# Optimization experiments

Measured on AMD Instinct MI355X. Metric: run time of the kernel, lower is better.

The kernel has to match this reference:

```python
import jax, jax.numpy as jnp
import numpy as np


def _ln(x, g, b):
    m = x.mean(-1, keepdims=True)
    v = x.var(-1, keepdims=True)
    return (x - m) * jax.lax.rsqrt(v + 1e-5) * g + b


def _shift(x):
    # RWKV time-shift: xx[t] = x[t-1], xx[0] = 0
    return jnp.pad(x, ((0, 0), (1, 0), (0, 0)))[:, :-1]


def setup_inputs() -> dict:
    key = jax.random.key(0)
    ks = jax.random.split(key, 20)
    B, S, D, E, F = 2, 2048, 1024, 8, 2048
    s = 0.02
    return dict(
        x=jax.random.normal(ks[0], (B, S, D), jnp.float32),
        ln1_g=jnp.ones((D,), jnp.float32), ln1_b=jnp.zeros((D,), jnp.float32),
        ln2_g=jnp.ones((D,), jnp.float32), ln2_b=jnp.zeros((D,), jnp.float32),
        tm_mu_k=jax.random.uniform(ks[1], (D,), jnp.float32),
        tm_mu_v=jax.random.uniform(ks[2], (D,), jnp.float32),
        tm_mu_r=jax.random.uniform(ks[3], (D,), jnp.float32),
        time_decay=jax.random.normal(ks[4], (D,), jnp.float32) * 0.1,
        time_first=jax.random.normal(ks[5], (D,), jnp.float32) * 0.1,
        Wk=jax.random.normal(ks[6], (D, D), jnp.float32) * s,
        Wv=jax.random.normal(ks[7], (D, D), jnp.float32) * s,
        Wr=jax.random.normal(ks[8], (D, D), jnp.float32) * s,
        Wo=jax.random.normal(ks[9], (D, D), jnp.float32) * s,
        router_w=jax.random.normal(ks[10], (D, E), jnp.float32) * s,
        cm_mu_k=jax.random.uniform(ks[11], (E, D), jnp.float32),
        cm_mu_r=jax.random.uniform(ks[12], (E, D), jnp.float32),
        eWk=jax.random.normal(ks[13], (E, D, F), jnp.float32) * s,
        eWv=jax.random.normal(ks[14], (E, F, D), jnp.float32) * s,
        eWr=jax.random.normal(ks[15], (E, D, D), jnp.float32) * s,
    )


def reference(x, ln1_g, ln1_b, ln2_g, ln2_b, tm_mu_k, tm_mu_v, tm_mu_r,
              time_decay, time_first, Wk, Wv, Wr, Wo, router_w,
              cm_mu_k, cm_mu_r, eWk, eWv, eWr):
    TOP_K = 2
    E = router_w.shape[1]
    B, S, D = x.shape

    # ---- TimeMix on ln1(x) ----
    xn = _ln(x, ln1_g, ln1_b)
    xx = _shift(xn)
    xk = xn * tm_mu_k + xx * (1.0 - tm_mu_k)
    xv = xn * tm_mu_v + xx * (1.0 - tm_mu_v)
    xr = xn * tm_mu_r + xx * (1.0 - tm_mu_r)
    k = xk @ Wk  # [B,S,D]
    v = xv @ Wv
    r = jax.nn.sigmoid(xr @ Wr)

    w = -jnp.exp(time_decay)  # per-channel decay < 0
    u = time_first

    def step(carry, kv_t):
        aa, bb, pp = carry
        kt, vt = kv_t
        qq = jnp.maximum(pp, u + kt)
        e1 = jnp.exp(pp - qq)
        e2 = jnp.exp(u + kt - qq)
        wkv_t = (e1 * aa + e2 * vt) / (e1 * bb + e2)
        qq2 = jnp.maximum(pp + w, kt)
        e1b = jnp.exp(pp + w - qq2)
        e2b = jnp.exp(kt - qq2)
        return (e1b * aa + e2b * vt, e1b * bb + e2b, qq2), wkv_t

    init = (jnp.zeros((B, D), x.dtype), jnp.zeros((B, D), x.dtype),
            jnp.full((B, D), -1e30, x.dtype))
    _, wkv = jax.lax.scan(step, init,
                          (k.transpose(1, 0, 2), v.transpose(1, 0, 2)))
    wkv = wkv.transpose(1, 0, 2)  # [B,S,D]
    x = x + (r * wkv) @ Wo  # residual

    # ---- Router on ln2(x) ----
    ei = _ln(x, ln2_g, ln2_b)
    probs = jax.nn.softmax(ei @ router_w, axis=-1)  # [B,S,E]
    vals, idx = jax.lax.top_k(probs, TOP_K)
    wts = vals / vals.sum(-1, keepdims=True)
    # dense per-token per-expert combine weight [B,S,E]
    tw = jnp.sum(jax.nn.one_hot(idx, E, dtype=x.dtype) * wts[..., None], axis=-2)

    # ---- Dense per-expert ChannelMix (every expert over full tensor) ----
    exx = _shift(ei)
    mk = cm_mu_k[:, None, None, :]  # [E,1,1,D]
    mr = cm_mu_r[:, None, None, :]
    xk_e = ei[None] * mk + exx[None] * (1.0 - mk)  # [E,B,S,D]
    xr_e = ei[None] * mr + exx[None] * (1.0 - mr)
    k_e = jnp.square(jax.nn.relu(jnp.einsum('ebsd,edf->ebsf', xk_e, eWk)))
    kv_e = jnp.einsum('ebsf,efd->ebsd', k_e, eWv)
    r_e = jax.nn.sigmoid(jnp.einsum('ebsd,edg->ebsg', xr_e, eWr))
    expert_out = r_e * kv_e  # [E,B,S,D]
    moe = jnp.einsum('ebsd,bse->bsd', expert_out, tw)
    return x + moe
```

## Files before the change

kernel.cpp:

```cpp
#include <hip/hip_runtime.h>
#include <hip/hip_bf16.h>
#include <stdint.h>

#define DEVI __device__ __forceinline__

typedef __attribute__((ext_vector_type(4))) float f32x4;
typedef __attribute__((ext_vector_type(8))) short short8;
typedef __attribute__((ext_vector_type(4))) short s16x4;

constexpr int B_ = 2, S_ = 2048, D_ = 1024, E_ = 8, F_ = 2048;
constexpr int M_ = B_ * S_;
constexpr int PC_ = 10240;
constexpr int NC_ = 64, L_ = 32;
constexpr int HB_ = 16;
constexpr size_t MD_ = (size_t)M_ * D_;
constexpr size_t DD_ = (size_t)D_ * D_;

DEVI short f2bf(float f) {
  uint32_t u = __float_as_uint(f);
  u = (u + 0x7fffu + ((u >> 16) & 1u)) >> 16;
  return (short)u;
}
DEVI float bf2f(short s) { return __uint_as_float(((uint32_t)(uint16_t)s) << 16); }
struct BfPair { short hi, lo; };
DEVI BfPair split2(float f) {
  BfPair p;
  p.hi = f2bf(f);
  p.lo = f2bf(f - bf2f(p.hi));
  return p;
}

DEVI void gload_lds16(const void* g, void* l) {
  __builtin_amdgcn_global_load_lds(
      (const __attribute__((address_space(1))) unsigned int*)g,
      (__attribute__((address_space(3))) unsigned int*)l, 16, 0, 0);
}

DEVI int swz(int row, int slot) { return slot ^ ((row >> 1) & 3); }

#define MFMA(a, b, c) __builtin_amdgcn_mfma_f32_16x16x32_bf16((a), (b), (c), 0, 0, 0)

__global__ __launch_bounds__(256) void lnmix_kernel(
    const float* __restrict__ x, const float* __restrict__ g,
    const float* __restrict__ b, const float* __restrict__ muk,
    const float* __restrict__ muv, const float* __restrict__ mur,
    short* __restrict__ xk, short* __restrict__ xv, short* __restrict__ xr) {
  int row = blockIdx.x;
  int tx = threadIdx.x;
  int s = row & (S_ - 1);
  size_t o = (size_t)row * D_ + tx * 4;
  f32x4 cur = *(const f32x4*)(x + o);
  f32x4 prv = {0.f, 0.f, 0.f, 0.f};
  if (s > 0) prv = *(const f32x4*)(x + o - D_);
  float a0 = cur[0] + cur[1] + cur[2] + cur[3];
  float a1 = cur[0] * cur[0] + cur[1] * cur[1] + cur[2] * cur[2] + cur[3] * cur[3];
  float a2 = prv[0] + prv[1] + prv[2] + prv[3];
  float a3 = prv[0] * prv[0] + prv[1] * prv[1] + prv[2] * prv[2] + prv[3] * prv[3];
#pragma unroll
  for (int o2 = 32; o2; o2 >>= 1) {
    a0 += __shfl_down(a0, o2);
    a1 += __shfl_down(a1, o2);
    a2 += __shfl_down(a2, o2);
    a3 += __shfl_down(a3, o2);
  }
  __shared__ float rd[4][4];
  if ((tx & 63) == 0) {
    rd[tx >> 6][0] = a0; rd[tx >> 6][1] = a1;
    rd[tx >> 6][2] = a2; rd[tx >> 6][3] = a3;
  }
  __syncthreads();
  a0 = rd[0][0] + rd[1][0] + rd[2][0] + rd[3][0];
  a1 = rd[0][1] + rd[1][1] + rd[2][1] + rd[3][1];
  a2 = rd[0][2] + rd[1][2] + rd[2][2] + rd[3][2];
  a3 = rd[0][3] + rd[1][3] + rd[2][3] + rd[3][3];
  float mc = a0 * (1.0f / D_);
  float rc = rsqrtf(a1 * (1.0f / D_) - mc * mc + 1e-5f);
  float mp = a2 * (1.0f / D_);
  float rp = rsqrtf(a3 * (1.0f / D_) - mp * mp + 1e-5f);
  int d = tx * 4;
  f32x4 gg = *(const f32x4*)(g + d);
  f32x4 bb = *(const f32x4*)(b + d);
  f32x4 mk = *(const f32x4*)(muk + d);
  f32x4 mv = *(const f32x4*)(muv + d);
  f32x4 mr = *(const f32x4*)(mur + d);
  s16x4 okh, okl, ovh, ovl, orh, orl;
#pragma unroll
  for (int j = 0; j < 4; j++) {
    float c = (cur[j] - mc) * rc * gg[j] + bb[j];
    float p = (s > 0) ? (prv[j] - mp) * rp * gg[j] + bb[j] : 0.f;
    BfPair pk = split2(c * mk[j] + p * (1.f - mk[j]));
    BfPair pv = split2(c * mv[j] + p * (1.f - mv[j]));
    BfPair pr = split2(c * mr[j] + p * (1.f - mr[j]));
    okh[j] = pk.hi; okl[j] = pk.lo;
    ovh[j] = pv.hi; ovl[j] = pv.lo;
    orh[j] = pr.hi; orl[j] = pr.lo;
  }
  *(s16x4*)(xk + o) = okh;
  *(s16x4*)(xk + MD_ + o) = okl;
  *(s16x4*)(xv + o) = ovh;
  *(s16x4*)(xv + MD_ + o) = ovl;
  *(s16x4*)(xr + o) = orh;
  *(s16x4*)(xr + MD_ + o) = orl;
}

__global__ __launch_bounds__(256) void ln2_router(
    const float* __restrict__ x, const float* __restrict__ P,
    const float* __restrict__ g, const float* __restrict__ b,
    const float* __restrict__ rw, float* __restrict__ xout,
    float* __restrict__ ei, int* __restrict__ idx2, float* __restrict__ wts2) {
  int row = blockIdx.x;
  int tx = threadIdx.x;
  size_t o = (size_t)row * D_ + tx * 4;
  f32x4 v = *(const f32x4*)(x + o);
  f32x4 p0 = *(const f32x4*)(P + o);
  f32x4 p1 = *(const f32x4*)(P + MD_ + o);
#pragma unroll
  for (int j = 0; j < 4; j++) v[j] += p0[j] + p1[j];
  *(f32x4*)(xout + o) = v;
  float s = v[0] + v[1] + v[2] + v[3];
  float s2 = v[0] * v[0] + v[1] * v[1] + v[2] * v[2] + v[3] * v[3];
#pragma unroll
  for (int of = 32; of; of >>= 1) {
    s += __shfl_down(s, of);
    s2 += __shfl_down(s2, of);
  }
  __shared__ float w1[4], w2[4];
  if ((tx & 63) == 0) { w1[tx >> 6] = s; w2[tx >> 6] = s2; }
  __syncthreads();
  s = w1[0] + w1[1] + w1[2] + w1[3];
  s2 = w2[0] + w2[1] + w2[2] + w2[3];
  float mean = s * (1.0f / D_);
  float rstd = rsqrtf(s2 * (1.0f / D_) - mean * mean + 1e-5f);
  f32x4 gg = *(const f32x4*)(g + tx * 4);
  f32x4 bb = *(const f32x4*)(b + tx * 4);
  f32x4 oo;
#pragma unroll
  for (int j = 0; j < 4; j++) oo[j] = (v[j] - mean) * rstd * gg[j] + bb[j];
  *(f32x4*)(ei + o) = oo;
  float pl[8] = {};
  const float* rr = rw + (size_t)(tx * 4) * 8;
#pragma unroll
  for (int j = 0; j < 4; j++)
#pragma unroll
    for (int e = 0; e < 8; e++) pl[e] += oo[j] * rr[j * 8 + e];
#pragma unroll
  for (int of = 32; of; of >>= 1)
#pragma unroll
    for (int e = 0; e < 8; e++) pl[e] += __shfl_down(pl[e], of);
  __shared__ float plw[4][8];
  if ((tx & 63) == 0)
#pragma unroll
    for (int e = 0; e < 8; e++) plw[tx >> 6][e] = pl[e];
  __syncthreads();
  if (tx == 0) {
    float p8[8];
#pragma unroll
    for (int e = 0; e < 8; e++)
      p8[e] = plw[0][e] + plw[1][e] + plw[2][e] + plw[3][e];
    float mx = p8[0];
#pragma unroll
    for (int e = 1; e < 8; e++) mx = fmaxf(mx, p8[e]);
    float pr[8];
#pragma unroll
    for (int e = 0; e < 8; e++) pr[e] = __expf(p8[e] - mx);
    int i1 = 0;
#pragma unroll
    for (int e = 1; e < 8; e++)
      if (pr[e] > pr[i1]) i1 = e;
    int i2 = (i1 == 0) ? 1 : 0;
#pragma unroll
    for (int e = 0; e < 8; e++)
      if (e != i1 && pr[e] > pr[i2]) i2 = e;
    float v1 = pr[i1], v2 = pr[i2];
    float inv = 1.f / (v1 + v2);
    int t = row;
    idx2[t * 2] = i1;
    idx2[t * 2 + 1] = i2;
    wts2[t * 2] = v1 * inv;
    wts2[t * 2 + 1] = v2 * inv;
  }
}

__global__ __launch_bounds__(512) void hist_kernel(const int* __restrict__ idx2,
                                                   int* __restrict__ pos2,
                                                   int* __restrict__ blockcnt) {
  __shared__ int cnt[8];
  int tx = threadIdx.x;
  if (tx < 8) cnt[tx] = 0;
  __syncthreads();
  int entry = blockIdx.x * 512 + tx;
  int e = idx2[entry];
  pos2[entry] = atomicAdd(&cnt[e], 1);
  __syncthreads();
  if (tx < 8) blockcnt[blockIdx.x * 8 + tx] = cnt[tx];
}

__global__ __launch_bounds__(128) void scan_kernel(const int* __restrict__ blockcnt,
                                                   int* __restrict__ offs,
                                                   int* __restrict__ counts,
                                                   int* __restrict__ gbase) {
  __shared__ int c[HB_][8];
  __shared__ int tot[8];
  __shared__ int eoff[9];
  int tx = threadIdx.x;
  c[tx >> 3][tx & 7] = blockcnt[tx];
  __syncthreads();
  if (tx < 8) {
    int s = 0;
    for (int b2 = 0; b2 < HB_; b2++) {
      int v = c[b2][tx];
      c[b2][tx] = s;
      s += v;
    }
    tot[tx] = s;
    counts[tx] = s;
  }
  __syncthreads();
  if (tx == 0) {
    int o = 0;
    for (int e = 0; e < 8; e++) {
      eoff[e] = o;
      o += ((tot[e] + 255) >> 8) << 8;
    }
    eoff[8] = o;
    for (int e = 0; e < 9; e++) offs[e] = eoff[e];
  }
  __syncthreads();
  gbase[tx] = eoff[tx & 7] + c[tx >> 3][tx & 7];
}

__global__ __launch_bounds__(256) void slot_kernel(const int* __restrict__ idx2,
                                                   const int* __restrict__ pos2,
                                                   const int* __restrict__ gbase,
                                                   int* __restrict__ elist,
                                                   int* __restrict__ slots) {
  int entry = blockIdx.x * 256 + threadIdx.x;
  int e = idx2[entry];
  int slot = gbase[(entry >> 9) * 8 + e] + pos2[entry];
  elist[slot] = entry >> 1;
  slots[entry] = slot;
}

template <int SPLIT>
__global__ __launch_bounds__(256) void transpose_cvt(const float* __restrict__ in,
                                                     short* __restrict__ out, int R,
                                                     int C) {
  __shared__ float t[32][33];
  size_t PS = (size_t)R * C;
  const float* inm = in + (size_t)blockIdx.z * PS;
  short* outm = out + (size_t)blockIdx.z * PS * (SPLIT ? 2 : 1);
  int r = threadIdx.x >> 3;
  int c4 = (threadIdx.x & 7) * 4;
  f32x4 v = *(const f32x4*)(inm + (size_t)(blockIdx.y * 32 + r) * C + blockIdx.x * 32 + c4);
#pragma unroll
  for (int i = 0; i < 4; i++) t[r][c4 + i] = v[i];
  __syncthreads();
  s16x4 oh, ol;
#pragma unroll
  for (int i = 0; i < 4; i++) {
    float val = t[c4 + i][r];
    if (SPLIT) {
      BfPair p = split2(val);
      oh[i] = p.hi;
      ol[i] = p.lo;
    } else {
      oh[i] = f2bf(val);
    }
  }
  size_t oidx = (size_t)(blockIdx.x * 32 + r) * R + blockIdx.y * 32 + c4;
  *(s16x4*)(outm + oidx) = oh;
  if (SPLIT) *(s16x4*)(outm + PS + oidx) = ol;
}

__global__ __launch_bounds__(256) void transpose_cvt4(
    const float* __restrict__ w0, const float* __restrict__ w1,
    const float* __restrict__ w2, const float* __restrict__ w3,
    short* __restrict__ out) {
  __shared__ float t[32][33];
  int z = blockIdx.z;
  const float* inm = (z == 0) ? w0 : (z == 1) ? w1 : (z == 2) ? w2 : w3;
  short* outm = out + (size_t)z * (2 * DD_);
  int r = threadIdx.x >> 3;
  int c4 = (threadIdx.x & 7) * 4;
  f32x4 v = *(const f32x4*)(inm + (size_t)(blockIdx.y * 32 + r) * D_ + blockIdx.x * 32 + c4);
#pragma unroll
  for (int i = 0; i < 4; i++) t[r][c4 + i] = v[i];
  __syncthreads();
  s16x4 oh, ol;
#pragma unroll
  for (int i = 0; i < 4; i++) {
    BfPair p = split2(t[c4 + i][r]);
    oh[i] = p.hi;
    ol[i] = p.lo;
  }
  size_t oidx = (size_t)(blockIdx.x * 32 + r) * D_ + blockIdx.y * 32 + c4;
  *(s16x4*)(outm + oidx) = oh;
  *(s16x4*)(outm + DD_ + oidx) = ol;
}


__global__ __launch_bounds__(512) void gemm_kvr(const short* __restrict__ X,
                                                const short* __restrict__ W,
                                                float* __restrict__ KVR) {
  __shared__ __align__(16) short Ah[256 * 32], Al[256 * 32];
  __shared__ __align__(16) short Bh[128 * 32], Bl[128 * 32];
  int tx = threadIdx.x;
  int lane = tx & 63;
  int orig = blockIdx.x + (blockIdx.y << 3) + (blockIdx.z << 7);
  int wgid = (orig & 7) * 48 + (orig >> 3);
  int z = wgid >> 7;
  int rem = wgid & 127;
  int colStart = (rem & 7) * 128;
  int rowStart = (rem >> 3) * 256;
  const short* A0 = X + (size_t)z * (2 * MD_) + (size_t)rowStart * D_;
  const short* B0 = W + (size_t)z * (2 * DD_) + (size_t)colStart * D_;
  float* C = KVR + (size_t)z * MD_;
  int wave = tx >> 6, wm = wave >> 1, wn = wave & 1;
  f32x4 acc[4][4] = {};
  for (int k0 = 0; k0 < D_; k0 += 32) {
#pragma unroll
    for (int i = 0; i < 2; i++) {
      int c = i * 512 + tx;
      int row = c >> 2;
      int kb = swz(row, c & 3) * 16;
      size_t go = (size_t)row * (D_ * 2) + (size_t)k0 * 2 + kb;
      size_t lo = (size_t)(i * 512 + (tx & ~63)) * 16;
      gload_lds16((const char*)A0 + go, (char*)Ah + lo);
      gload_lds16((const char*)A0 + MD_ * 2 + go, (char*)Al + lo);
    }
    {
      int row = tx >> 2;
      int kb = swz(row, tx & 3) * 16;
      size_t go = (size_t)row * (D_ * 2) + (size_t)k0 * 2 + kb;
      size_t lo = (size_t)(tx & ~63) * 16;
      gload_lds16((const char*)B0 + go, (char*)Bh + lo);
      gload_lds16((const char*)B0 + DD_ * 2 + go, (char*)Bl + lo);
    }
    __syncthreads();
    short8 a[4], a2[4], b[4], b2[4];
#pragma unroll
    for (int m = 0; m < 4; m++) {
      int rr_ = wm * 64 + m * 16 + (lane & 15);
      int ro = rr_ * 32 + swz(rr_, lane >> 4) * 8;
      a[m] = *(const short8*)(Ah + ro);
      a2[m] = *(const short8*)(Al + ro);
    }
#pragma unroll
    for (int n = 0; n < 4; n++) {
      int rr_ = wn * 64 + n * 16 + (lane & 15);
      int ro = rr_ * 32 + swz(rr_, lane >> 4) * 8;
      b[n] = *(const short8*)(Bh + ro);
      b2[n] = *(const short8*)(Bl + ro);
    }
#pragma unroll
    for (int m = 0; m < 4; m++)
#pragma unroll
      for (int n = 0; n < 4; n++) {
        acc[m][n] = MFMA(a[m], b[n], acc[m][n]);
        acc[m][n] = MFMA(a2[m], b[n], acc[m][n]);
        acc[m][n] = MFMA(a[m], b2[n], acc[m][n]);
      }
    __syncthreads();
  }
  int r0 = rowStart + wm * 64 + ((lane >> 4) << 2);
  int cgl = colStart + wn * 64 + (lane & 15);
#pragma unroll
  for (int m = 0; m < 4; m++)
#pragma unroll
    for (int n = 0; n < 4; n++)
#pragma unroll
      for (int j = 0; j < 4; j++) {
        size_t idx = (size_t)(r0 + m * 16 + j) * D_ + cgl + n * 16;
        float vv = acc[m][n][j];
        if (z == 2) vv = 1.0f / (1.0f + __expf(-vv));
        C[idx] = vv;
      }
}

__global__ __launch_bounds__(512) void gemm_wo(const short* __restrict__ A,
                                               const short* __restrict__ Bt,
                                               float* __restrict__ P) {
  __shared__ __align__(16) short Ah[256 * 32], Al[256 * 32];
  __shared__ __align__(16) short Bh[128 * 32], Bl[128 * 32];
  int tx = threadIdx.x;
  int lane = tx & 63;
  int orig = blockIdx.x + (blockIdx.y << 3) + (blockIdx.z << 7);
  int wgid = (orig & 7) * 32 + (orig >> 3);
  int z = wgid >> 7;
  int rem = wgid & 127;
  int colStart = (rem & 7) * 128;
  int rowStart = (rem >> 3) * 256;
  const short* A0 = A + (size_t)rowStart * D_;
  const short* B0 = Bt + (size_t)colStart * D_;
  float* C = P + (size_t)z * MD_;
  int wave = tx >> 6, wm = wave >> 1, wn = wave & 1;
  f32x4 acc[4][4] = {};
  int kbase = z * (D_ / 2);
  for (int k0 = kbase; k0 < kbase + D_ / 2; k0 += 32) {
#pragma unroll
    for (int i = 0; i < 2; i++) {
      int c = i * 512 + tx;
      int row = c >> 2;
      int kb = swz(row, c & 3) * 16;
      size_t go = (size_t)row * (D_ * 2) + (size_t)k0 * 2 + kb;
      size_t lo = (size_t)(i * 512 + (tx & ~63)) * 16;
      gload_lds16((const char*)A0 + go, (char*)Ah + lo);
      gload_lds16((const char*)A0 + MD_ * 2 + go, (char*)Al + lo);
    }
    {
      int row = tx >> 2;
      int kb = swz(row, tx & 3) * 16;
      size_t go = (size_t)row * (D_ * 2) + (size_t)k0 * 2 + kb;
      size_t lo = (size_t)(tx & ~63) * 16;
      gload_lds16((const char*)B0 + go, (char*)Bh + lo);
      gload_lds16((const char*)B0 + DD_ * 2 + go, (char*)Bl + lo);
    }
    __syncthreads();
    short8 a[4], a2[4], b[4], b2[4];
#pragma unroll
    for (int m = 0; m < 4; m++) {
      int rr_ = wm * 64 + m * 16 + (lane & 15);
      int ro = rr_ * 32 + swz(rr_, lane >> 4) * 8;
      a[m] = *(const short8*)(Ah + ro);
      a2[m] = *(const short8*)(Al + ro);
    }
#pragma unroll
    for (int n = 0; n < 4; n++) {
      int rr_ = wn * 64 + n * 16 + (lane & 15);
      int ro = rr_ * 32 + swz(rr_, lane >> 4) * 8;
      b[n] = *(const short8*)(Bh + ro);
      b2[n] = *(const short8*)(Bl + ro);
    }
#pragma unroll
    for (int m = 0; m < 4; m++)
#pragma unroll
      for (int n = 0; n < 4; n++) {
        acc[m][n] = MFMA(a[m], b[n], acc[m][n]);
        acc[m][n] = MFMA(a2[m], b[n], acc[m][n]);
        acc[m][n] = MFMA(a[m], b2[n], acc[m][n]);
      }
    __syncthreads();
  }
  int r0 = rowStart + wm * 64 + ((lane >> 4) << 2);
  int cgl = colStart + wn * 64 + (lane & 15);
#pragma unroll
  for (int m = 0; m < 4; m++)
#pragma unroll
    for (int n = 0; n < 4; n++)
#pragma unroll
      for (int j = 0; j < 4; j++)
        C[(size_t)(r0 + m * 16 + j) * D_ + cgl + n * 16] = acc[m][n][j];
}

__global__ __launch_bounds__(512) void gemm_exA(const short* __restrict__ A,
                                                const short* __restrict__ Bt,
                                                short* __restrict__ C,
                                                const int* __restrict__ offs) {
  __shared__ __align__(16) short As[2][256 * 32];
  __shared__ __align__(16) short Bs[2][128 * 32];
  int tx = threadIdx.x;
  int lane = tx & 63;
  int orig = blockIdx.x + (blockIdx.y << 4);
  int wgid = (orig & 7) * 80 + (orig >> 3);
  int colStart = (wgid & 15) * 128;
  int rowStart = (wgid >> 4) * 256;
  if (rowStart >= offs[8]) return;
  int e = 0;
  while (e < 7 && rowStart >= offs[e + 1]) e++;
  const char* Ag = (const char*)(A + (size_t)rowStart * D_);
  const char* Bg = (const char*)(Bt + (size_t)e * F_ * D_ + (size_t)colStart * D_);
  int wave = tx >> 6, wm = wave >> 1, wn = wave & 1;
  auto stage = [&](int buf, int s) {
    size_t kb2 = (size_t)s << 6;
#pragma unroll
    for (int i = 0; i < 2; i++) {
      int c = i * 512 + tx;
      int row = c >> 2;
      int kb = swz(row, c & 3) * 16;
      gload_lds16(Ag + (size_t)row * (D_ * 2) + kb2 + kb,
                  (char*)As[buf] + (size_t)(i * 512 + (tx & ~63)) * 16);
    }
    {
      int row = tx >> 2;
      int kb = swz(row, tx & 3) * 16;
      gload_lds16(Bg + (size_t)row * (D_ * 2) + kb2 + kb,
                  (char*)Bs[buf] + (size_t)(tx & ~63) * 16);
    }
  };
  f32x4 acc[4][4] = {};
  constexpr int NS = 32;
  int cur = 0;
  stage(0, 0);
  for (int s = 0; s < NS; s++) {
    if (s + 1 < NS) {
      stage(cur ^ 1, s + 1);
      asm volatile("s_waitcnt vmcnt(3)" ::: "memory");
    } else {
      asm volatile("s_waitcnt vmcnt(0)" ::: "memory");
    }
    __builtin_amdgcn_s_barrier();
    short8 a[4], b[4];
#pragma unroll
    for (int m = 0; m < 4; m++) {
      int rr_ = wm * 64 + m * 16 + (lane & 15);
      a[m] = *(const short8*)(As[cur] + rr_ * 32 + swz(rr_, lane >> 4) * 8);
    }
#pragma unroll
    for (int n = 0; n < 4; n++) {
      int rr_ = wn * 64 + n * 16 + (lane & 15);
      b[n] = *(const short8*)(Bs[cur] + rr_ * 32 + swz(rr_, lane >> 4) * 8);
    }
    __builtin_amdgcn_s_setprio(1);
#pragma unroll
    for (int m = 0; m < 4; m++)
#pragma unroll
      for (int n = 0; n < 4; n++) acc[m][n] = MFMA(a[m], b[n], acc[m][n]);
    __builtin_amdgcn_s_setprio(0);
    asm volatile("" ::: "memory");
    __builtin_amdgcn_s_barrier();
    cur ^= 1;
  }
  int r0 = rowStart + wm * 64 + ((lane >> 4) << 2);
  int cgl = colStart + wn * 64 + (lane & 15);
#pragma unroll
  for (int m = 0; m < 4; m++)
#pragma unroll
    for (int n = 0; n < 4; n++)
#pragma unroll
      for (int j = 0; j < 4; j++) {
        size_t idx = (size_t)(r0 + m * 16 + j) * F_ + cgl + n * 16;
        float vv = acc[m][n][j];
        vv = vv > 0.f ? vv * vv : 0.f;
        C[idx] = f2bf(vv);
      }
}

__global__ __launch_bounds__(512) void gemm_ex2(
    const short* __restrict__ h, const short* __restrict__ eWvT,
    short* __restrict__ kvb, const short* __restrict__ Ar,
    const short* __restrict__ eWrT, short* __restrict__ rrb,
    const int* __restrict__ offs) {
  __shared__ __align__(16) short As[2][256 * 32];
  __shared__ __align__(16) short Bs[2][128 * 32];
  int tx = threadIdx.x;
  int lane = tx & 63;
  int zz = blockIdx.z;
  int orig = blockIdx.x + (blockIdx.y << 3);
  int wgid = (orig & 7) * 40 + (orig >> 3);
  int colStart = (wgid & 7) * 128;
  int rowStart = (wgid >> 3) * 256;
  if (rowStart >= offs[8]) return;
  int e = 0;
  while (e < 7 && rowStart >= offs[e + 1]) e++;
  int K = zz ? D_ : F_;
  const char* Ag = (const char*)((zz ? Ar : h) + (size_t)rowStart * K);
  const char* Bg =
      (const char*)((zz ? eWrT : eWvT) + (size_t)e * D_ * K + (size_t)colStart * K);
  int wave = tx >> 6, wm = wave >> 1, wn = wave & 1;
  const int NS = K / 32;
  auto stage = [&](int buf, int s) {
    size_t kb2 = (size_t)s << 6;
#pragma unroll
    for (int i = 0; i < 2; i++) {
      int c = i * 512 + tx;
      int row = c >> 2;
      int kb = swz(row, c & 3) * 16;
      gload_lds16(Ag + (size_t)row * ((size_t)K * 2) + kb2 + kb,
                  (char*)As[buf] + (size_t)(i * 512 + (tx & ~63)) * 16);
    }
    {
      int row = tx >> 2;
      int kb = swz(row, tx & 3) * 16;
      gload_lds16(Bg + (size_t)row * ((size_t)K * 2) + kb2 + kb,
                  (char*)Bs[buf] + (size_t)(tx & ~63) * 16);
    }
  };
  f32x4 acc[4][4] = {};
  int cur = 0;
  stage(0, 0);
  for (int s = 0; s < NS; s++) {
    if (s + 1 < NS) {
      stage(cur ^ 1, s + 1);
      asm volatile("s_waitcnt vmcnt(3)" ::: "memory");
    } else {
      asm volatile("s_waitcnt vmcnt(0)" ::: "memory");
    }
    __builtin_amdgcn_s_barrier();
    short8 a[4], b[4];
#pragma unroll
    for (int m = 0; m < 4; m++) {
      int rr_ = wm * 64 + m * 16 + (lane & 15);
      a[m] = *(const short8*)(As[cur] + rr_ * 32 + swz(rr_, lane >> 4) * 8);
    }
#pragma unroll
    for (int n = 0; n < 4; n++) {
      int rr_ = wn * 64 + n * 16 + (lane & 15);
      b[n] = *(const short8*)(Bs[cur] + rr_ * 32 + swz(rr_, lane >> 4) * 8);
    }
    __builtin_amdgcn_s_setprio(1);
#pragma unroll
    for (int m = 0; m < 4; m++)
#pragma unroll
      for (int n = 0; n < 4; n++) acc[m][n] = MFMA(a[m], b[n], acc[m][n]);
    __builtin_amdgcn_s_setprio(0);
    asm volatile("" ::: "memory");
    __builtin_amdgcn_s_barrier();
    cur ^= 1;
  }
  short* C = zz ? rrb : kvb;
  int r0 = rowStart + wm * 64 + ((lane >> 4) << 2);
  int cgl = colStart + wn * 64 + (lane & 15);
#pragma unroll
  for (int m = 0; m < 4; m++)
#pragma unroll
    for (int n = 0; n < 4; n++)
#pragma unroll
      for (int j = 0; j < 4; j++) {
        size_t idx = (size_t)(r0 + m * 16 + j) * D_ + cgl + n * 16;
        float vv = acc[m][n][j];
        if (zz) vv = 1.0f / (1.0f + __expf(-vv));
        C[idx] = f2bf(vv);
      }
}

__global__ __launch_bounds__(256) void wkv_chunk_kernel(const float* __restrict__ k,
                                                        const float* __restrict__ v,
                                                        const float* __restrict__ td,
                                                        float* __restrict__ chA,
                                                        float* __restrict__ chB) {
  int d = blockIdx.x * 256 + threadIdx.x;
  int c = blockIdx.y;
  int b = blockIdx.z;
  float w = -__expf(td[d]);
  float dec = __expf(w);
  float A = 0.f, Bb = 0.f;
  size_t base = ((size_t)b * S_ + (size_t)c * L_) * D_ + d;
  for (int i = 0; i < L_; i++) {
    float kt = k[base + (size_t)i * D_];
    float vt = v[base + (size_t)i * D_];
    float ek = __expf(kt);
    A = fmaf(A, dec, ek * vt);
    Bb = fmaf(Bb, dec, ek);
  }
  size_t o = ((size_t)b * NC_ + c) * D_ + d;
  chA[o] = A;
  chB[o] = Bb;
}

__global__ __launch_bounds__(256) void wkv_carry_kernel(const float* __restrict__ chA,
                                                        const float* __restrict__ chB,
                                                        const float* __restrict__ td,
                                                        float* __restrict__ caA,
                                                        float* __restrict__ caB) {
  int d = blockIdx.x * 256 + threadIdx.x;
  int b = blockIdx.y;
  float w = -__expf(td[d]);
  float decL = __expf(w * (float)L_);
  float A = 0.f, Bb = 0.f;
  for (int c = 0; c < NC_; c++) {
    size_t o = ((size_t)b * NC_ + c) * D_ + d;
    caA[o] = A;
    caB[o] = Bb;
    A = fmaf(A, decL, chA[o]);
    Bb = fmaf(Bb, decL, chB[o]);
  }
}

__global__ __launch_bounds__(256) void wkv_out_kernel(
    const float* __restrict__ k, const float* __restrict__ v,
    const float* __restrict__ r, const float* __restrict__ caA,
    const float* __restrict__ caB, const float* __restrict__ td,
    const float* __restrict__ tf, short* __restrict__ rwkv) {
  int d = blockIdx.x * 256 + threadIdx.x;
  int c = blockIdx.y;
  int b = blockIdx.z;
  float w = -__expf(td[d]);
  float dec = __expf(w);
  float eu = __expf(tf[d]);
  size_t co = ((size_t)b * NC_ + c) * D_ + d;
  float A = caA[co], Bb = caB[co];
  size_t base = ((size_t)b * S_ + (size_t)c * L_) * D_ + d;
  for (int i = 0; i < L_; i++) {
    size_t ix = base + (size_t)i * D_;
    float kt = k[ix], vt = v[ix], rt = r[ix];
    float ek = __expf(kt);
    float euk = eu * ek;
    float wkv = (A + euk * vt) / (Bb + euk);
    BfPair p = split2(rt * wkv);
    rwkv[ix] = p.hi;
    rwkv[MD_ + ix] = p.lo;
    A = fmaf(A, dec, ek * vt);
    Bb = fmaf(Bb, dec, ek);
  }
}

__global__ __launch_bounds__(256) void gather_mix_kernel(
    const float* __restrict__ ei, const float* __restrict__ cmk,
    const float* __restrict__ cmr, const int* __restrict__ offs,
    const int* __restrict__ counts, const int* __restrict__ elist,
    short* __restrict__ Ak, short* __restrict__ Ar) {
  int row = blockIdx.x;
  if (row >= offs[8]) return;
  int e = 0;
  while (e < 7 && row >= offs[e + 1]) e++;
  int p = row - offs[e];
  int d = threadIdx.x * 4;
  size_t ro = (size_t)row * D_ + d;
  if (p >= counts[e]) {
    s16x4 z = {0, 0, 0, 0};
    *(s16x4*)(Ak + ro) = z;
    *(s16x4*)(Ar + ro) = z;
    return;
  }
  int t = elist[row];
  int s = t & (S_ - 1);
  f32x4 cur = *(const f32x4*)(ei + (size_t)t * D_ + d);
  f32x4 prev = {0.f, 0.f, 0.f, 0.f};
  if (s > 0) prev = *(const f32x4*)(ei + (size_t)(t - 1) * D_ + d);
  f32x4 mk = *(const f32x4*)(cmk + (size_t)e * D_ + d);
  f32x4 mr = *(const f32x4*)(cmr + (size_t)e * D_ + d);
  s16x4 ok, orr;
#pragma unroll
  for (int j = 0; j < 4; j++) {
    ok[j] = f2bf(cur[j] * mk[j] + prev[j] * (1.f - mk[j]));
    orr[j] = f2bf(cur[j] * mr[j] + prev[j] * (1.f - mr[j]));
  }
  *(s16x4*)(Ak + ro) = ok;
  *(s16x4*)(Ar + ro) = orr;
}

__global__ __launch_bounds__(256) void final_kernel(
    const float* __restrict__ xout, const short* __restrict__ rrb,
    const short* __restrict__ kvb, const int* __restrict__ slots,
    const float* __restrict__ wts2, float* __restrict__ out) {
  size_t i4 = (size_t)blockIdx.x * 256 + threadIdx.x;
  size_t el = i4 * 4;
  int t = (int)(el >> 10);
  int d = (int)(el & (D_ - 1));
  int s0 = slots[t * 2], s1 = slots[t * 2 + 1];
  float w0 = wts2[t * 2], w1 = wts2[t * 2 + 1];
  f32x4 xo = *(const f32x4*)(xout + el);
  s16x4 r0 = *(const s16x4*)(rrb + (size_t)s0 * D_ + d);
  s16x4 k0 = *(const s16x4*)(kvb + (size_t)s0 * D_ + d);
  s16x4 r1 = *(const s16x4*)(rrb + (size_t)s1 * D_ + d);
  s16x4 k1 = *(const s16x4*)(kvb + (size_t)s1 * D_ + d);
  f32x4 o;
#pragma unroll
  for (int j = 0; j < 4; j++)
    o[j] = xo[j] + w0 * bf2f(r0[j]) * bf2f(k0[j]) + w1 * bf2f(r1[j]) * bf2f(k1[j]);
  *(f32x4*)(out + el) = o;
}

extern "C" void kernel_launch(void* const* d_in, const int* in_sizes, int n_in,
                              void* d_out, int out_size, void* d_ws, size_t ws_size,
                              hipStream_t stream) {
  (void)in_sizes; (void)n_in; (void)out_size; (void)ws_size;
  const float* x = (const float*)d_in[0];
  const float* ln1g = (const float*)d_in[1];
  const float* ln1b = (const float*)d_in[2];
  const float* ln2g = (const float*)d_in[3];
  const float* ln2b = (const float*)d_in[4];
  const float* muk = (const float*)d_in[5];
  const float* muv = (const float*)d_in[6];
  const float* mur = (const float*)d_in[7];
  const float* tdec = (const float*)d_in[8];
  const float* tfirst = (const float*)d_in[9];
  const float* Wk = (const float*)d_in[10];
  const float* Wv = (const float*)d_in[11];
  const float* Wr = (const float*)d_in[12];
  const float* Wo = (const float*)d_in[13];
  const float* rw = (const float*)d_in[14];
  const float* cmk = (const float*)d_in[15];
  const float* cmr = (const float*)d_in[16];
  const float* eWk = (const float*)d_in[17];
  const float* eWv = (const float*)d_in[18];
  const float* eWr = (const float*)d_in[19];
  float* out = (float*)d_out;

  char* w = (char*)d_ws;
  size_t off = 0;
  auto alloc = [&](size_t bytes) {
    size_t o = off;
    off = (off + bytes + 255) & ~(size_t)255;
    return o;
  };
  const size_t szDD2x2 = DD_ * 2 * 2;
  size_t o_WT = alloc(4 * szDD2x2);
  size_t o_WkT = o_WT, o_WoT = o_WT + 3 * szDD2x2;
  size_t o_eWkT = alloc((size_t)E_ * D_ * F_ * 2);
  size_t o_eWvT = alloc((size_t)E_ * F_ * D_ * 2);
  size_t o_eWrT = alloc((size_t)E_ * D_ * D_ * 2);
  size_t o_xout = alloc(MD_ * 4);
  size_t o_ei = alloc(MD_ * 4);
  size_t o_counts = alloc(64);
  size_t o_offs = alloc(64);
  size_t o_idx2 = alloc((size_t)M_ * 2 * 4);
  size_t o_wts2 = alloc((size_t)M_ * 2 * 4);
  size_t o_pos2 = alloc((size_t)M_ * 2 * 4);
  size_t o_blockcnt = alloc((size_t)HB_ * 8 * 4);
  size_t o_gbase = alloc((size_t)HB_ * 8 * 4);
  size_t o_elist = alloc((size_t)PC_ * 4);
  size_t o_slots = alloc((size_t)M_ * 2 * 4);
  size_t poolBase = off;
  size_t off1 = poolBase;
  auto alloc1 = [&](size_t bytes) {
    size_t o = off1;
    off1 = (off1 + bytes + 255) & ~(size_t)255;
    return o;
  };
  size_t o_rwkv = alloc1(MD_ * 2 * 2);
  size_t o_xk = alloc1(MD_ * 2 * 2);
  size_t o_xv = alloc1(MD_ * 2 * 2);
  size_t o_xr = alloc1(MD_ * 2 * 2);
  size_t o_k = alloc1(MD_ * 4);
  size_t o_v = alloc1(MD_ * 4);
  size_t o_r = alloc1(MD_ * 4);
  size_t o_chA = alloc1((size_t)B_ * NC_ * D_ * 4);
  size_t o_chB = alloc1((size_t)B_ * NC_ * D_ * 4);
  size_t o_caA = alloc1((size_t)B_ * NC_ * D_ * 4);
  size_t o_caB = alloc1((size_t)B_ * NC_ * D_ * 4);
  size_t o_P = o_k;
  size_t off2 = poolBase;
  auto alloc2 = [&](size_t bytes) {
    size_t o = off2;
    off2 = (off2 + bytes + 255) & ~(size_t)255;
    return o;
  };
  size_t o_Ak = alloc2((size_t)PC_ * D_ * 2);
  size_t o_Ar = alloc2((size_t)PC_ * D_ * 2);
  size_t o_h = alloc2((size_t)PC_ * F_ * 2);
  size_t o_kvb = alloc2((size_t)PC_ * D_ * 2);
  size_t o_rrb = alloc2((size_t)PC_ * D_ * 2);

#define WP(T, o) ((T*)(w + (o)))

  transpose_cvt4<<<dim3(32, 32, 4), 256, 0, stream>>>(Wk, Wv, Wr, Wo,
                                                      WP(short, o_WkT));
  transpose_cvt<0><<<dim3(F_ / 32, D_ / 32, E_), 256, 0, stream>>>(eWk, WP(short, o_eWkT), D_, F_);
  transpose_cvt<0><<<dim3(D_ / 32, F_ / 32, E_), 256, 0, stream>>>(eWv, WP(short, o_eWvT), F_, D_);
  transpose_cvt<0><<<dim3(D_ / 32, D_ / 32, E_), 256, 0, stream>>>(eWr, WP(short, o_eWrT), D_, D_);

  lnmix_kernel<<<M_, 256, 0, stream>>>(x, ln1g, ln1b, muk, muv, mur,
                                       WP(short, o_xk), WP(short, o_xv),
                                       WP(short, o_xr));

  gemm_kvr<<<dim3(8, 16, 3), 512, 0, stream>>>(WP(short, o_xk), WP(short, o_WkT),
                                               WP(float, o_k));

  wkv_chunk_kernel<<<dim3(D_ / 256, NC_, B_), 256, 0, stream>>>(
      WP(float, o_k), WP(float, o_v), tdec, WP(float, o_chA), WP(float, o_chB));
  wkv_carry_kernel<<<dim3(D_ / 256, B_), 256, 0, stream>>>(
      WP(float, o_chA), WP(float, o_chB), tdec, WP(float, o_caA), WP(float, o_caB));
  wkv_out_kernel<<<dim3(D_ / 256, NC_, B_), 256, 0, stream>>>(
      WP(float, o_k), WP(float, o_v), WP(float, o_r), WP(float, o_caA),
      WP(float, o_caB), tdec, tfirst, WP(short, o_rwkv));

  gemm_wo<<<dim3(8, 16, 2), 512, 0, stream>>>(WP(short, o_rwkv), WP(short, o_WoT),
                                              WP(float, o_P));
  ln2_router<<<M_, 256, 0, stream>>>(x, WP(float, o_P), ln2g, ln2b, rw,
                                     WP(float, o_xout), WP(float, o_ei),
                                     WP(int, o_idx2), WP(float, o_wts2));

  hist_kernel<<<HB_, 512, 0, stream>>>(WP(int, o_idx2), WP(int, o_pos2),
                                       WP(int, o_blockcnt));
  scan_kernel<<<1, 128, 0, stream>>>(WP(int, o_blockcnt), WP(int, o_offs),
                                     WP(int, o_counts), WP(int, o_gbase));
  slot_kernel<<<(2 * M_) / 256, 256, 0, stream>>>(WP(int, o_idx2), WP(int, o_pos2),
                                                  WP(int, o_gbase), WP(int, o_elist),
                                                  WP(int, o_slots));
  gather_mix_kernel<<<PC_, 256, 0, stream>>>(WP(float, o_ei), cmk, cmr, WP(int, o_offs),
                                             WP(int, o_counts), WP(int, o_elist),
                                             WP(short, o_Ak), WP(short, o_Ar));

  gemm_exA<<<dim3(16, 40), 512, 0, stream>>>(WP(short, o_Ak), WP(short, o_eWkT),
                                             WP(short, o_h), WP(int, o_offs));
  gemm_ex2<<<dim3(8, 40, 2), 512, 0, stream>>>(
      WP(short, o_h), WP(short, o_eWvT), WP(short, o_kvb), WP(short, o_Ar),
      WP(short, o_eWrT), WP(short, o_rrb), WP(int, o_offs));

  final_kernel<<<M_ * D_ / 4 / 256, 256, 0, stream>>>(
      WP(float, o_xout), WP(short, o_rrb), WP(short, o_kvb), WP(int, o_slots),
      WP(float, o_wts2), out);
#undef WP
}
```

Measured before the change: 437.4 us.

## Double-buffer split-bf16 GEMMs by streaming hi/lo terms as separate K stages

The gemm_kvr and gemm_wo kernels previously loaded the hi and lo bf16 halves of A and B together into single LDS buffers and synchronised twice per k-step. They now treat the three split-precision product terms (hi*hi, lo*hi, hi*lo) as separate stages along K. Each stage loads one A tile and one B tile into a double-buffered LDS slot while the previous slot is being computed, using vmcnt waits and raw barriers, and raises wave priority around the MFMA block. This is meant to overlap global-to-LDS loads with matrix math and cut LDS footprint per stage, at the cost of three times as many loop iterations and barriers.

```diff
diff --git a/kernel.cpp b/kernel.cpp
--- a/kernel.cpp
+++ b/kernel.cpp
@@ -302,8 +302,8 @@
 __global__ __launch_bounds__(512) void gemm_kvr(const short* __restrict__ X,
                                                 const short* __restrict__ W,
                                                 float* __restrict__ KVR) {
-  __shared__ __align__(16) short Ah[256 * 32], Al[256 * 32];
-  __shared__ __align__(16) short Bh[128 * 32], Bl[128 * 32];
+  __shared__ __align__(16) short As[2][256 * 32];
+  __shared__ __align__(16) short Bs[2][128 * 32];
   int tx = threadIdx.x;
   int lane = tx & 63;
   int orig = blockIdx.x + (blockIdx.y << 3) + (blockIdx.z << 7);
@@ -312,55 +312,62 @@
   int rem = wgid & 127;
   int colStart = (rem & 7) * 128;
   int rowStart = (rem >> 3) * 256;
-  const short* A0 = X + (size_t)z * (2 * MD_) + (size_t)rowStart * D_;
-  const short* B0 = W + (size_t)z * (2 * DD_) + (size_t)colStart * D_;
+  const char* A0 = (const char*)(X + (size_t)z * (2 * MD_) + (size_t)rowStart * D_);
+  const char* B0 = (const char*)(W + (size_t)z * (2 * DD_) + (size_t)colStart * D_);
   float* C = KVR + (size_t)z * MD_;
   int wave = tx >> 6, wm = wave >> 1, wn = wave & 1;
-  f32x4 acc[4][4] = {};
-  for (int k0 = 0; k0 < D_; k0 += 32) {
+  auto stage = [&](int buf, int s) {
+    int term = s >> 5;
+    size_t kb2 = (size_t)(s & 31) << 6;
+    const char* Ap = A0 + (size_t)(term == 1 ? 1 : 0) * (MD_ * 2);
+    const char* Bp = B0 + (size_t)(term == 2 ? 1 : 0) * (DD_ * 2);
 #pragma unroll
     for (int i = 0; i < 2; i++) {
       int c = i * 512 + tx;
       int row = c >> 2;
       int kb = swz(row, c & 3) * 16;
-      size_t go = (size_t)row * (D_ * 2) + (size_t)k0 * 2 + kb;
-      size_t lo = (size_t)(i * 512 + (tx & ~63)) * 16;
-      gload_lds16((const char*)A0 + go, (char*)Ah + lo);
-      gload_lds16((const char*)A0 + MD_ * 2 + go, (char*)Al + lo);
+      gload_lds16(Ap + (size_t)row * (D_ * 2) + kb2 + kb,
+                  (char*)As[buf] + (size_t)(i * 512 + (tx & ~63)) * 16);
     }
     {
       int row = tx >> 2;
       int kb = swz(row, tx & 3) * 16;
-      size_t go = (size_t)row * (D_ * 2) + (size_t)k0 * 2 + kb;
-      size_t lo = (size_t)(tx & ~63) * 16;
-      gload_lds16((const char*)B0 + go, (char*)Bh + lo);
-      gload_lds16((const char*)B0 + DD_ * 2 + go, (char*)Bl + lo);
-    }
-    __syncthreads();
-    short8 a[4], a2[4], b[4], b2[4];
+      gload_lds16(Bp + (size_t)row * (D_ * 2) + kb2 + kb,
+                  (char*)Bs[buf] + (size_t)(tx & ~63) * 16);
+    }
+  };
+  f32x4 acc[4][4] = {};
+  constexpr int NS = 96;
+  int cur = 0;
+  stage(0, 0);
+  for (int s = 0; s < NS; s++) {
+    if (s + 1 < NS) {
+      stage(cur ^ 1, s + 1);
+      asm volatile("s_waitcnt vmcnt(3)" ::: "memory");
+    } else {
+      asm volatile("s_waitcnt vmcnt(0)" ::: "memory");
+    }
+    __builtin_amdgcn_s_barrier();
+    short8 a[4], b[4];
 #pragma unroll
     for (int m = 0; m < 4; m++) {
       int rr_ = wm * 64 + m * 16 + (lane & 15);
-      int ro = rr_ * 32 + swz(rr_, lane >> 4) * 8;
-      a[m] = *(const short8*)(Ah + ro);
-      a2[m] = *(const short8*)(Al + ro);
+      a[m] = *(const short8*)(As[cur] + rr_ * 32 + swz(rr_, lane >> 4) * 8);
     }
 #pragma unroll
     for (int n = 0; n < 4; n++) {
       int rr_ = wn * 64 + n * 16 + (lane & 15);
-      int ro = rr_ * 32 + swz(rr_, lane >> 4) * 8;
-      b[n] = *(const short8*)(Bh + ro);
-      b2[n] = *(const short8*)(Bl + ro);
-    }
+      b[n] = *(const short8*)(Bs[cur] + rr_ * 32 + swz(rr_, lane >> 4) * 8);
+    }
+    __builtin_amdgcn_s_setprio(1);
 #pragma unroll
     for (int m = 0; m < 4; m++)
 #pragma unroll
-      for (int n = 0; n < 4; n++) {
-        acc[m][n] = MFMA(a[m], b[n], acc[m][n]);
-        acc[m][n] = MFMA(a2[m], b[n], acc[m][n]);
-        acc[m][n] = MFMA(a[m], b2[n], acc[m][n]);
-      }
-    __syncthreads();
+      for (int n = 0; n < 4; n++) acc[m][n] = MFMA(a[m], b[n], acc[m][n]);
+    __builtin_amdgcn_s_setprio(0);
+    asm volatile("" ::: "memory");
+    __builtin_amdgcn_s_barrier();
+    cur ^= 1;
   }
   int r0 = rowStart + wm * 64 + ((lane >> 4) << 2);
   int cgl = colStart + wn * 64 + (lane & 15);
@@ -380,8 +387,8 @@
 __global__ __launch_bounds__(512) void gemm_wo(const short* __restrict__ A,
                                                const short* __restrict__ Bt,
                                                float* __restrict__ P) {
-  __shared__ __align__(16) short Ah[256 * 32], Al[256 * 32];
-  __shared__ __align__(16) short Bh[128 * 32], Bl[128 * 32];
+  __shared__ __align__(16) short As[2][256 * 32];
+  __shared__ __align__(16) short Bs[2][128 * 32];
   int tx = threadIdx.x;
   int lane = tx & 63;
   int orig = blockIdx.x + (blockIdx.y << 3) + (blockIdx.z << 7);
@@ -390,56 +397,63 @@
   int rem = wgid & 127;
   int colStart = (rem & 7) * 128;
   int rowStart = (rem >> 3) * 256;
-  const short* A0 = A + (size_t)rowStart * D_;
-  const short* B0 = Bt + (size_t)colStart * D_;
+  const char* A0 = (const char*)(A + (size_t)rowStart * D_);
+  const char* B0 = (const char*)(Bt + (size_t)colStart * D_);
   float* C = P + (size_t)z * MD_;
   int wave = tx >> 6, wm = wave >> 1, wn = wave & 1;
-  f32x4 acc[4][4] = {};
-  int kbase = z * (D_ / 2);
-  for (int k0 = kbase; k0 < kbase + D_ / 2; k0 += 32) {
+  size_t kbase = (size_t)z * 1024;
+  auto stage = [&](int buf, int s) {
+    int term = s >> 4;
+    size_t kb2 = kbase + ((size_t)(s & 15) << 6);
+    const char* Ap = A0 + (size_t)(term == 1 ? 1 : 0) * (MD_ * 2);
+    const char* Bp = B0 + (size_t)(term == 2 ? 1 : 0) * (DD_ * 2);
 #pragma unroll
     for (int i = 0; i < 2; i++) {
       int c = i * 512 + tx;
       int row = c >> 2;
       int kb = swz(row, c & 3) * 16;
-      size_t go = (size_t)row * (D_ * 2) + (size_t)k0 * 2 + kb;
-      size_t lo = (size_t)(i * 512 + (tx & ~63)) * 16;
-      gload_lds16((const char*)A0 + go, (char*)Ah + lo);
-      gload_lds16((const char*)A0 + MD_ * 2 + go, (char*)Al + lo);
+      gload_lds16(Ap + (size_t)row * (D_ * 2) + kb2 + kb,
+                  (char*)As[buf] + (size_t)(i * 512 + (tx & ~63)) * 16);
     }
     {
       int row = tx >> 2;
       int kb = swz(row, tx & 3) * 16;
-      size_t go = (size_t)row * (D_ * 2) + (size_t)k0 * 2 + kb;
-      size_t lo = (size_t)(tx & ~63) * 16;
-      gload_lds16((const char*)B0 + go, (char*)Bh + lo);
-      gload_lds16((const char*)B0 + DD_ * 2 + go, (char*)Bl + lo);
-    }
-    __syncthreads();
-    short8 a[4], a2[4], b[4], b2[4];
+      gload_lds16(Bp + (size_t)row * (D_ * 2) + kb2 + kb,
+                  (char*)Bs[buf] + (size_t)(tx & ~63) * 16);
+    }
+  };
+  f32x4 acc[4][4] = {};
+  constexpr int NS = 48;
+  int cur = 0;
+  stage(0, 0);
+  for (int s = 0; s < NS; s++) {
+    if (s + 1 < NS) {
+      stage(cur ^ 1, s + 1);
+      asm volatile("s_waitcnt vmcnt(3)" ::: "memory");
+    } else {
+      asm volatile("s_waitcnt vmcnt(0)" ::: "memory");
+    }
+    __builtin_amdgcn_s_barrier();
+    short8 a[4], b[4];
 #pragma unroll
     for (int m = 0; m < 4; m++) {
       int rr_ = wm * 64 + m * 16 + (lane & 15);
-      int ro = rr_ * 32 + swz(rr_, lane >> 4) * 8;
-      a[m] = *(const short8*)(Ah + ro);
-      a2[m] = *(const short8*)(Al + ro);
+      a[m] = *(const short8*)(As[cur] + rr_ * 32 + swz(rr_, lane >> 4) * 8);
     }
 #pragma unroll
     for (int n = 0; n < 4; n++) {
       int rr_ = wn * 64 + n * 16 + (lane & 15);
-      int ro = rr_ * 32 + swz(rr_, lane >> 4) * 8;
-      b[n] = *(const short8*)(Bh + ro);
-      b2[n] = *(const short8*)(Bl + ro);
-    }
+      b[n] = *(const short8*)(Bs[cur] + rr_ * 32 + swz(rr_, lane >> 4) * 8);
+    }
+    __builtin_amdgcn_s_setprio(1);
 #pragma unroll
     for (int m = 0; m < 4; m++)
 #pragma unroll
-      for (int n = 0; n < 4; n++) {
-        acc[m][n] = MFMA(a[m], b[n], acc[m][n]);
-        acc[m][n] = MFMA(a2[m], b[n], acc[m][n]);
-        acc[m][n] = MFMA(a[m], b2[n], acc[m][n]);
-      }
-    __syncthreads();
+      for (int n = 0; n < 4; n++) acc[m][n] = MFMA(a[m], b[n], acc[m][n]);
+    __builtin_amdgcn_s_setprio(0);
+    asm volatile("" ::: "memory");
+    __builtin_amdgcn_s_barrier();
+    cur ^= 1;
   }
   int r0 = rowStart + wm * 64 + ((lane >> 4) << 2);
   int cgl = colStart + wn * 64 + (lane & 15);
```

New measurement: 456.6 us. 4.4% more time.
